# Optimization experiments

Hardware: AMD Instinct MI355X
Metric: run time of the kernel (lower is better)

## Reference

```python
import jax, jax.numpy as jnp
import numpy as np

H, W = 256, 192           # cfg.input_img_shape
INF = 9999.0
B, V = 64, 100000


def setup_inputs() -> dict:
    key = jax.random.key(0)
    k1, k2, k3 = jax.random.split(key, 3)
    sdf = jax.random.normal(k1, (B, V), dtype=jnp.float32)
    # pixel coords spanning slightly beyond the image so some verts are invalid
    uv = jax.random.uniform(k2, (B, V, 2), dtype=jnp.float32)
    cloth_meshes = uv * jnp.array([W * 1.1, H * 1.1], jnp.float32) - jnp.array([W * 0.05, H * 0.05], jnp.float32)
    parse_gt = jax.random.randint(k3, (B, H, W), 0, 2).astype(jnp.int32)
    return {
        "sdf": sdf,
        "cloth_meshes": cloth_meshes,
        "parse_gt": parse_gt,
        "sdf_thresh": jnp.ones((1,), jnp.float32),
        "cloth_meshes_unposed": jnp.zeros((1, 1, 3), jnp.float32),
        "parse_valid": jnp.ones((B, 1, 1), jnp.float32),
        "dist_thresh": jnp.ones((1,), jnp.float32),
        "v_template": jnp.zeros((1, 3), jnp.float32),
    }


def reference(sdf, cloth_meshes, parse_gt, sdf_thresh, cloth_meshes_unposed, parse_valid, dist_thresh, v_template):
    b = sdf.shape[0]
    hw = H * W
    x = cloth_meshes[:, :, 0].astype(jnp.int32)
    y = cloth_meshes[:, :, 1].astype(jnp.int32)
    is_valid = (x >= 0) & (x < W) & (y >= 0) & (y < H)
    idx = jnp.where(is_valid, y * W + x, 0)                      # [B,V]
    min_sdf = jnp.where(is_valid, sdf, INF)
    max_sdf = jnp.where(is_valid, sdf, -INF)
    # single flattened segment reduce over B*H*W segments (scatter_min/max)
    flat_idx = (idx + jnp.arange(b, dtype=jnp.int32)[:, None] * hw).reshape(-1)
    pmin = jax.ops.segment_min(min_sdf.reshape(-1), flat_idx, num_segments=b * hw).reshape(b, H, W)
    pmax = jax.ops.segment_max(max_sdf.reshape(-1), flat_idx, num_segments=b * hw).reshape(b, H, W)
    # empty / all-invalid pixels: torch init was +/-INF -> replace
    pmin = jnp.where(pmin >= INF, 0.0, pmin)
    pmax = jnp.where(pmax <= -INF, sdf_thresh[0], pmax)
    pos_mask = (parse_gt == 1).astype(sdf.dtype)
    neg_mask = (parse_gt == 0).astype(sdf.dtype)
    loss_pos = jnp.abs(pmin) * pos_mask * parse_valid
    loss_neg = jnp.abs(pmax - sdf_thresh[0]) * neg_mask * parse_valid
    loss = loss_pos.mean((1, 2)) + loss_neg.mean((1, 2))
    cloth_exist = (pos_mask.sum((1, 2)) > 0).astype(sdf.dtype)
    return loss * cloth_exist
```

## Files before the change

### kernel.cpp

```cpp
#include <hip/hip_runtime.h>


#define HH 256
#define WW 192
#define HW (HH * WW)
#define NB 64
#define NV 100000
#define NS 4
#define RANGE (HW / NS)
#define NC 8
#define CHUNK (NV / NC)
#define F4B (NV / 4 / NC)
#define CAP 3000

__device__ __forceinline__ unsigned fkey(float f) {
    unsigned u = __float_as_uint(f);
    return (u & 0x80000000u) ? ~u : (u | 0x80000000u);
}
__device__ __forceinline__ float funkey(unsigned k) {
    unsigned u = (k & 0x80000000u) ? (k ^ 0x80000000u) : ~k;
    return __uint_as_float(u);
}
__device__ __forceinline__ unsigned key18(float f) {
    unsigned k = fkey(f);
    if (k >= 0xFFFFE000u) return 0x3FFFFu;
    return (k + 0x2000u) >> 14;
}

__global__ __launch_bounds__(512) void bin_kernel(
        const float4* __restrict__ sdf4,
        const float4* __restrict__ mesh4,
        unsigned* __restrict__ cnt,
        unsigned* __restrict__ records) {
    __shared__ unsigned lcur[NS];
    const int b = blockIdx.x >> 3;
    const int c = blockIdx.x & 7;
    const int tid = threadIdx.x;
    if (tid < NS) lcur[tid] = 0;
    __syncthreads();

    const float4* sbase = sdf4  + (size_t)b * (NV / 4) + (size_t)c * F4B;
    const float4* mbase = mesh4 + (size_t)b * (NV / 2) + (size_t)c * F4B * 2;
    unsigned* rbase = records + (size_t)(b * NC + c) * NS * CAP;

    for (int g = tid; g < F4B; g += 512) {
        float4 s4 = sbase[g];
        float4 ma = mbase[2 * g];
        float4 mb = mbase[2 * g + 1];
        float xs[4] = {ma.x, ma.z, mb.x, mb.z};
        float ys[4] = {ma.y, ma.w, mb.y, mb.w};
        float ss[4] = {s4.x, s4.y, s4.z, s4.w};
        #pragma unroll
        for (int j = 0; j < 4; ++j) {
            int x = (int)xs[j];
            int y = (int)ys[j];
            if ((unsigned)x < WW && (unsigned)y < HH) {
                int q = y >> 6;
                unsigned pos = atomicAdd(&lcur[q], 1u);
                if (pos < CAP)
                    rbase[q * CAP + pos] =
                        ((unsigned)((y & 63) * WW + x) << 18) | key18(ss[j]);
            }
        }
    }
    __syncthreads();
    if (tid < NS) cnt[(b * NC + c) * NS + tid] = lcur[tid];
}

__global__ __launch_bounds__(1024) void scatter_reduce_kernel(
        const unsigned* __restrict__ records,
        const unsigned* __restrict__ cnt,
        const int4* __restrict__ gt4,
        const float* __restrict__ thr_p,
        float* __restrict__ sums,
        unsigned* __restrict__ counts) {
    __shared__ unsigned ldsk[RANGE];
    __shared__ unsigned char gtb[RANGE];
    const int b = blockIdx.x >> 2;
    const int q = blockIdx.x & 3;
    const int tid = threadIdx.x;

    int lpos = 0;
    for (int j = tid; j < RANGE; j += 1024) ldsk[j] = 0xFFFFFFFFu;
    const int4* gbase = gt4 + ((size_t)b * HW + (size_t)q * RANGE) / 4;
    for (int j = tid; j < RANGE / 4; j += 1024) {
        int4 g = gbase[j];
        gtb[4 * j + 0] = (unsigned char)g.x;
        gtb[4 * j + 1] = (unsigned char)g.y;
        gtb[4 * j + 2] = (unsigned char)g.z;
        gtb[4 * j + 3] = (unsigned char)g.w;
        lpos |= (g.x == 1) | (g.y == 1) | (g.z == 1) | (g.w == 1);
    }
    __syncthreads();

    for (int c = 0; c < NC; ++c) {
        unsigned n = cnt[(b * NC + c) * NS + q];
        if (n > CAP) n = CAP;
        const unsigned* rb = records + ((size_t)(b * NC + c) * NS + q) * CAP;
        for (unsigned i = tid; i < n; i += 1024) {
            unsigned r = rb[i];
            unsigned p = r >> 18;
            unsigned k = r & 0x3FFFFu;
            if (gtb[p] == 0) k ^= 0x3FFFFu;
            atomicMin(&ldsk[p], k);
        }
    }
    __syncthreads();

    const float thr = thr_p[0];
    float lsum = 0.f;
    for (int j = tid; j < RANGE; j += 1024) {
        unsigned k = ldsk[j];
        if (k <= 0x3FFFFu) {
            if (gtb[j]) lsum += fabsf(funkey(k << 14));
            else        lsum += fabsf(funkey((k ^ 0x3FFFFu) << 14) - thr);
        }
    }
    #pragma unroll
    for (int off = 32; off > 0; off >>= 1)
        lsum += __shfl_down(lsum, off, 64);
    unsigned long long m = __ballot(lpos != 0);
    if ((tid & 63) == 0) {
        atomicAdd(&sums[b], lsum);
        if (m) atomicOr(&counts[b], 1u);
    }
}

__global__ void final_kernel(const float* __restrict__ sums,
                             const unsigned* __restrict__ counts,
                             const float* __restrict__ pv,
                             float* __restrict__ out) {
    int b = threadIdx.x;
    if (b < NB) {
        float s = sums[b] * (1.0f / HW) * pv[b];
        out[b] = counts[b] ? s : 0.0f;
    }
}

extern "C" void kernel_launch(void* const* d_in, const int* in_sizes, int n_in,
                              void* d_out, int out_size, void* d_ws, size_t ws_size,
                              hipStream_t stream) {
    const float* sdf  = (const float*)d_in[0];
    const float* mesh = (const float*)d_in[1];
    const int*   gt   = (const int*)d_in[2];
    const float* thr  = (const float*)d_in[3];
    const float* pv   = (const float*)d_in[5];
    float* out = (float*)d_out;

    unsigned* cnt     = (unsigned*)d_ws;
    float*    sums    = (float*)((char*)d_ws + 8192);
    unsigned* counts  = (unsigned*)((char*)d_ws + 8448);
    unsigned* records = (unsigned*)((char*)d_ws + 8704);

    hipMemsetAsync(sums, 0, 512, stream);

    bin_kernel<<<NB * NC, 512, 0, stream>>>(
        (const float4*)sdf, (const float4*)mesh, cnt, records);

    scatter_reduce_kernel<<<NB * NS, 1024, 0, stream>>>(
        records, cnt, (const int4*)gt, thr, sums, counts);

    final_kernel<<<1, 64, 0, stream>>>(sums, counts, pv, out);
}
```

Before: 167.4 us.

## Double strip and chunk partitions and assign one wave per chunk with vector loads

Splits the image into 8 row strips and each batch's vertices into 16 chunks. This doubles the block count of both the binning and the scatter-reduce kernels, and the per-strip record capacity is cut to match. In the scatter-reduce kernel each of the 16 waves now handles one chunk's record list, reading it with 128-bit loads plus a scalar tail, instead of all threads walking the chunks one after another. The count array is transposed so a block's 16 counts are contiguous. The aim is more parallelism and better occupancy, with smaller LDS per block and fewer serialized loop iterations. The cost is a tighter capacity margin that could drop records if a strip overflows.

```diff
diff --git a/kernel.cpp b/kernel.cpp
--- a/kernel.cpp
+++ b/kernel.cpp
@@ -6,12 +6,11 @@
 #define HW (HH * WW)
 #define NB 64
 #define NV 100000
-#define NS 4
+#define NS 8
 #define RANGE (HW / NS)
-#define NC 8
-#define CHUNK (NV / NC)
-#define F4B (NV / 4 / NC)
-#define CAP 3000
+#define NC 16
+#define G4 (NV / 4)
+#define CAP 896
 
 __device__ __forceinline__ unsigned fkey(float f) {
     unsigned u = __float_as_uint(f);
@@ -33,17 +32,19 @@
         unsigned* __restrict__ cnt,
         unsigned* __restrict__ records) {
     __shared__ unsigned lcur[NS];
-    const int b = blockIdx.x >> 3;
-    const int c = blockIdx.x & 7;
+    const int b = blockIdx.x >> 4;
+    const int c = blockIdx.x & 15;
     const int tid = threadIdx.x;
     if (tid < NS) lcur[tid] = 0;
     __syncthreads();
 
-    const float4* sbase = sdf4  + (size_t)b * (NV / 4) + (size_t)c * F4B;
-    const float4* mbase = mesh4 + (size_t)b * (NV / 2) + (size_t)c * F4B * 2;
+    const int g0 = (c * G4) >> 4;
+    const int g1 = ((c + 1) * G4) >> 4;
+    const float4* sbase = sdf4  + (size_t)b * G4;
+    const float4* mbase = mesh4 + (size_t)b * G4 * 2;
     unsigned* rbase = records + (size_t)(b * NC + c) * NS * CAP;
 
-    for (int g = tid; g < F4B; g += 512) {
+    for (int g = g0 + tid; g < g1; g += 512) {
         float4 s4 = sbase[g];
         float4 ma = mbase[2 * g];
         float4 mb = mbase[2 * g + 1];
@@ -55,16 +56,16 @@
             int x = (int)xs[j];
             int y = (int)ys[j];
             if ((unsigned)x < WW && (unsigned)y < HH) {
-                int q = y >> 6;
+                int q = y >> 5;
                 unsigned pos = atomicAdd(&lcur[q], 1u);
                 if (pos < CAP)
                     rbase[q * CAP + pos] =
-                        ((unsigned)((y & 63) * WW + x) << 18) | key18(ss[j]);
+                        ((unsigned)((y & 31) * WW + x) << 18) | key18(ss[j]);
             }
         }
     }
     __syncthreads();
-    if (tid < NS) cnt[(b * NC + c) * NS + tid] = lcur[tid];
+    if (tid < NS) cnt[(b * NS + tid) * NC + c] = lcur[tid];
 }
 
 __global__ __launch_bounds__(1024) void scatter_reduce_kernel(
@@ -76,8 +77,8 @@
         unsigned* __restrict__ counts) {
     __shared__ unsigned ldsk[RANGE];
     __shared__ unsigned char gtb[RANGE];
-    const int b = blockIdx.x >> 2;
-    const int q = blockIdx.x & 3;
+    const int b = blockIdx.x >> 3;
+    const int q = blockIdx.x & 7;
     const int tid = threadIdx.x;
 
     int lpos = 0;
@@ -93,17 +94,30 @@
     }
     __syncthreads();
 
-    for (int c = 0; c < NC; ++c) {
-        unsigned n = cnt[(b * NC + c) * NS + q];
-        if (n > CAP) n = CAP;
-        const unsigned* rb = records + ((size_t)(b * NC + c) * NS + q) * CAP;
-        for (unsigned i = tid; i < n; i += 1024) {
-            unsigned r = rb[i];
-            unsigned p = r >> 18;
-            unsigned k = r & 0x3FFFFu;
+    const int wave = tid >> 6;
+    const int lane = tid & 63;
+    unsigned n = cnt[(b * NS + q) * NC + wave];
+    if (n > CAP) n = CAP;
+    const unsigned* rb = records + ((size_t)(b * NC + wave) * NS + q) * CAP;
+    const uint4* rb4 = (const uint4*)rb;
+    unsigned n4 = n >> 2;
+    for (unsigned i = lane; i < n4; i += 64) {
+        uint4 r = rb4[i];
+        unsigned ra[4] = {r.x, r.y, r.z, r.w};
+        #pragma unroll
+        for (int j = 0; j < 4; ++j) {
+            unsigned p = ra[j] >> 18;
+            unsigned k = ra[j] & 0x3FFFFu;
             if (gtb[p] == 0) k ^= 0x3FFFFu;
             atomicMin(&ldsk[p], k);
         }
+    }
+    for (unsigned i = (n4 << 2) + lane; i < n; i += 64) {
+        unsigned r = rb[i];
+        unsigned p = r >> 18;
+        unsigned k = r & 0x3FFFFu;
+        if (gtb[p] == 0) k ^= 0x3FFFFu;
+        atomicMin(&ldsk[p], k);
     }
     __syncthreads();
 
@@ -148,9 +162,9 @@
     float* out = (float*)d_out;
 
     unsigned* cnt     = (unsigned*)d_ws;
-    float*    sums    = (float*)((char*)d_ws + 8192);
-    unsigned* counts  = (unsigned*)((char*)d_ws + 8448);
-    unsigned* records = (unsigned*)((char*)d_ws + 8704);
+    float*    sums    = (float*)((char*)d_ws + 32768);
+    unsigned* counts  = (unsigned*)((char*)d_ws + 33024);
+    unsigned* records = (unsigned*)((char*)d_ws + 33280);
 
     hipMemsetAsync(sums, 0, 512, stream);
 
```

New measurement: 196.1 us. 1.17x slower.
